# Performance work log

Hardware: AMD Instinct MI355X
Metric: run time of the kernel (lower is better)

## Reference

```python
import jax, jax.numpy as jnp
import numpy as np

LN_EPS = 1e-5

def _layernorm(x, gamma, beta):
    # x: [B, 4, H]; gamma/beta: [4, H]; computed in fp32 as the torch subclass does
    x32 = x.astype(jnp.float32)
    mu = jnp.mean(x32, axis=-1, keepdims=True)
    var = jnp.mean(jnp.square(x32 - mu), axis=-1, keepdims=True)
    y = (x32 - mu) * jax.lax.rsqrt(var + LN_EPS)
    return (y * gamma + beta).astype(x.dtype)

def setup_inputs() -> dict:
    key = jax.random.key(0)
    ks = jax.random.split(key, 6)
    B, I, H = 8192, 512, 1024
    x = jax.random.normal(ks[0], (B, I), dtype=jnp.float32)
    h = jax.random.normal(ks[1], (B, H), dtype=jnp.float32)
    c = jax.random.normal(ks[2], (B, H), dtype=jnp.float32)
    Wi = jax.random.normal(ks[3], (I, 4 * H), dtype=jnp.float32) * (1.0 / np.sqrt(I))
    Wh = jax.random.normal(ks[4], (H, 4 * H), dtype=jnp.float32) * (1.0 / np.sqrt(H))
    bh = jax.random.normal(ks[5], (4 * H,), dtype=jnp.float32) * 0.01
    ln_gamma = jnp.ones((4, H), dtype=jnp.float32)
    ln_beta = jnp.zeros((4, H), dtype=jnp.float32)
    return {"x": x, "h": h, "c": c, "Wi": Wi, "Wh": Wh, "bh": bh,
            "ln_gamma": ln_gamma, "ln_beta": ln_beta}

def reference(x, h, c, Wi, Wh, bh, ln_gamma, ln_beta):
    B = x.shape[0]
    H = h.shape[-1]
    gates = x @ Wi + h @ Wh + bh            # [B, 4H]
    gates = gates.reshape(B, 4, H)           # chunk into i, f, g, o
    gates = _layernorm(gates, ln_gamma, ln_beta)
    i, f, g, o = gates[:, 0], gates[:, 1], gates[:, 2], gates[:, 3]
    c_new = jax.nn.sigmoid(f) * c + jax.nn.sigmoid(i) * jnp.tanh(g)
    h_new = jax.nn.sigmoid(o) * jnp.tanh(c_new)   # layer_norm_c is Identity
    return (h_new, c_new)
```

## Files before the change

### kernel.cpp

```cpp
#include <hip/hip_runtime.h>
#include <stdint.h>

#define BATCH 8192
#define IDIM  512
#define HDIM  1024
#define KDIM  1536
#define NDIM  4096
#define BK    32

typedef __bf16 bf16x8 __attribute__((ext_vector_type(8)));
typedef float  f32x4  __attribute__((ext_vector_type(4)));
typedef unsigned short u16x8 __attribute__((ext_vector_type(8)));

__device__ __forceinline__ unsigned short f2bf(float f) {
    union { float f; unsigned u; } v; v.f = f;
    unsigned r = v.u + 0x7fffu + ((v.u >> 16) & 1u);
    return (unsigned short)(r >> 16);
}
__device__ __forceinline__ float bf2f(unsigned short u) {
    union { unsigned u; float f; } v; v.u = ((unsigned)u) << 16;
    return v.f;
}
__device__ __forceinline__ float fexp(float x) {
    return __builtin_amdgcn_exp2f(x * 1.44269504f);
}
__device__ __forceinline__ float sigm(float x) {
    return __builtin_amdgcn_rcpf(1.f + fexp(-x));
}
__device__ __forceinline__ float ftanh(float x) {
    return 1.f - 2.f * __builtin_amdgcn_rcpf(1.f + fexp(2.f * x));
}

__device__ __forceinline__ void load16(void* lds, const void* g) {
    __builtin_amdgcn_global_load_lds(
        (const __attribute__((address_space(1))) unsigned int*)g,
        (__attribute__((address_space(3))) unsigned int*)lds, 16, 0, 0);
}

#define PACKA_BLKS (BATCH * KDIM / 8 / 512)
#define PACKW_BLKS ((NDIM / 64) * (KDIM / 32))
__global__ __launch_bounds__(512) void pack_ab(const float* __restrict__ x,
                                               const float* __restrict__ h,
                                               const float* __restrict__ Wi,
                                               const float* __restrict__ Wh,
                                               unsigned short* __restrict__ A,
                                               unsigned short* __restrict__ Wt) {
    __shared__ float tile[32][65];
    const int t   = threadIdx.x;
    const int blk = blockIdx.x;
    if (blk < PACKA_BLKS) {
        int idx = blk * 512 + t;
        int row = idx / (KDIM / 8);
        int g8  = idx % (KDIM / 8);
        const float* src = (g8 < IDIM / 8)
                         ? x + (size_t)row * IDIM + g8 * 8
                         : h + (size_t)row * HDIM + (g8 - IDIM / 8) * 8;
        float4 v0 = ((const float4*)src)[0];
        float4 v1 = ((const float4*)src)[1];
        u16x8 o;
        o[0] = f2bf(v0.x); o[1] = f2bf(v0.y); o[2] = f2bf(v0.z); o[3] = f2bf(v0.w);
        o[4] = f2bf(v1.x); o[5] = f2bf(v1.y); o[6] = f2bf(v1.z); o[7] = f2bf(v1.w);
        *(u16x8*)(A + (size_t)idx * 8) = o;
    } else {
        int b  = blk - PACKA_BLKS;
        int n0 = (b & 63) * 64;
        int k0 = (b >> 6) * 32;
        int tx = t & 63, ty = t >> 6;
#pragma unroll
        for (int j = 0; j < 4; j++) {
            int k = k0 + ty + 8 * j;
            float v;
            if (k < IDIM) v = Wi[(size_t)k * NDIM + n0 + tx];
            else          v = Wh[(size_t)(k - IDIM) * NDIM + n0 + tx];
            tile[ty + 8 * j][tx] = v;
        }
        __syncthreads();
        int nl = t >> 3, k4 = (t & 7) * 4;
        ushort4 o;
        o.x = f2bf(tile[k4 + 0][nl]);
        o.y = f2bf(tile[k4 + 1][nl]);
        o.z = f2bf(tile[k4 + 2][nl]);
        o.w = f2bf(tile[k4 + 3][nl]);
        *(ushort4*)(Wt + (size_t)(n0 + nl) * KDIM + k0 + k4) = o;
    }
}

__global__ __launch_bounds__(512, 2) void gemm_bt(const unsigned short* __restrict__ A,
                                                  const unsigned short* __restrict__ Bt,
                                                  unsigned short* __restrict__ C) {
    __shared__ __align__(16) unsigned short smem[65536];

    const int t    = threadIdx.x;
    const int wave = t >> 6;
    const int lane = t & 63;
    const int lrow = lane & 15;
    const int quad = lane >> 4;

    const int bid = blockIdx.x;
    const int xcd = bid & 7;
    const int jj  = bid >> 3;
    const int bm  = (xcd * 4 + (jj & 3)) * 256;
    const int bn  = (jj >> 2) * 256;

    const int wm = (wave & 1) * 128;
    const int wn = (wave >> 1) * 64;

    int srcA[2], srcB[2];
#pragma unroll
    for (int j = 0; j < 2; j++) {
        int q   = t + 512 * j;
        int rp  = q >> 3, s = q & 7;
        int xx  = s ^ (rp & 7);
        int row = 2 * rp + (xx >> 2);
        int kc  = xx & 3;
        srcA[j] = (bm + row) * KDIM + kc * 8;
        srcB[j] = (bn + row) * KDIM + kc * 8;
    }

    int offA[8], offB[4];
#pragma unroll
    for (int mt = 0; mt < 8; mt++) {
        int r = wm + mt * 16 + lrow;
        offA[mt] = (r >> 1) * 64 + (((((r & 1) << 2) | quad) ^ ((r >> 1) & 7)) * 8);
    }
#pragma unroll
    for (int nt = 0; nt < 4; nt++) {
        int r = wn + nt * 16 + lrow;
        offB[nt] = (r >> 1) * 64 + (((((r & 1) << 2) | quad) ^ ((r >> 1) & 7)) * 8);
    }

    f32x4 acc[8][4] = {};

#define STAGE(tt) do {                                              \
    unsigned short* _d = smem + (((tt) & 3) << 14);                 \
    const int _ko = (tt) * 32;                                      \
    load16(_d +          t * 8, A  + (size_t)(srcA[0] + _ko));      \
    load16(_d +  4096 +  t * 8, A  + (size_t)(srcA[1] + _ko));      \
    load16(_d +  8192 +  t * 8, Bt + (size_t)(srcB[0] + _ko));      \
    load16(_d + 12288 +  t * 8, Bt + (size_t)(srcB[1] + _ko));      \
} while (0)

    STAGE(0); STAGE(1); STAGE(2);

    const int NT = KDIM / 32;
    for (int T = 0; T < NT; ++T) {
        if (T < NT - 2)       asm volatile("s_waitcnt vmcnt(8)" ::: "memory");
        else if (T == NT - 2) asm volatile("s_waitcnt vmcnt(4)" ::: "memory");
        else                  asm volatile("s_waitcnt vmcnt(0)" ::: "memory");
        __builtin_amdgcn_s_barrier();
        asm volatile("" ::: "memory");

        const unsigned short* bufA = smem + ((T & 3) << 14);
        const unsigned short* bufB = bufA + 8192;

        bf16x8 a[4], b[4], a2[4];
#pragma unroll
        for (int i = 0; i < 4; i++) a[i] = *(const bf16x8*)(bufA + offA[i]);
#pragma unroll
        for (int i = 0; i < 4; i++) b[i] = *(const bf16x8*)(bufB + offB[i]);
        __builtin_amdgcn_sched_barrier(0);
        if (T + 3 < NT) STAGE(T + 3);
#pragma unroll
        for (int i = 0; i < 4; i++) a2[i] = *(const bf16x8*)(bufA + offA[4 + i]);
        __builtin_amdgcn_sched_barrier(0);

        __builtin_amdgcn_s_setprio(1);
#pragma unroll
        for (int mt = 0; mt < 4; mt++)
#pragma unroll
            for (int nt = 0; nt < 4; nt++)
                acc[mt][nt] = __builtin_amdgcn_mfma_f32_16x16x32_bf16(
                    a[mt], b[nt], acc[mt][nt], 0, 0, 0);
        __builtin_amdgcn_sched_barrier(0);

#pragma unroll
        for (int mt = 0; mt < 4; mt++)
#pragma unroll
            for (int nt = 0; nt < 4; nt++)
                acc[4 + mt][nt] = __builtin_amdgcn_mfma_f32_16x16x32_bf16(
                    a2[mt], b[nt], acc[4 + mt][nt], 0, 0, 0);
        __builtin_amdgcn_s_setprio(0);
        asm volatile("" ::: "memory");
    }
#undef STAGE

#pragma unroll
    for (int mt = 0; mt < 8; mt++)
#pragma unroll
        for (int nt = 0; nt < 4; nt++) {
            int row = bm + wm + mt * 16 + quad * 4;
            int col = bn + wn + nt * 16 + lrow;
#pragma unroll
            for (int r = 0; r < 4; r++)
                C[(size_t)(row + r) * NDIM + col] = f2bf(acc[mt][nt][r]);
        }
}

__global__ __launch_bounds__(512) void lstm_ep(const unsigned short* __restrict__ gates,
                                               const float* __restrict__ bh,
                                               const float* __restrict__ c,
                                               const float* __restrict__ gamma,
                                               const float* __restrict__ beta,
                                               float* __restrict__ out) {
    const int wave = threadIdx.x >> 6;
    const int lane = threadIdx.x & 63;
    const int b    = blockIdx.x * 8 + wave;
    const int col0 = lane * 16;

    const unsigned short* gr = gates + (size_t)b * NDIM;
    float v[4][16];
    float s[4], sq[4];
#pragma unroll
    for (int g = 0; g < 4; g++) {
        const unsigned short* gp = gr + g * HDIM + col0;
        u16x8 ga = *(const u16x8*)gp;
        u16x8 gb = *(const u16x8*)(gp + 8);
        float bb[16];
#pragma unroll
        for (int q = 0; q < 4; q++)
            *(float4*)(bb + 4 * q) = ((const float4*)(bh + g * HDIM + col0))[q];
        float ls = 0.f, lq = 0.f;
#pragma unroll
        for (int j = 0; j < 16; j++) {
            float tv = bf2f(j < 8 ? ga[j] : gb[j - 8]) + bb[j];
            v[g][j] = tv; ls += tv; lq += tv * tv;
        }
        s[g] = ls; sq[g] = lq;
    }
#pragma unroll
    for (int off = 32; off; off >>= 1) {
#pragma unroll
        for (int g = 0; g < 4; g++) {
            s[g]  += __shfl_xor(s[g], off);
            sq[g] += __shfl_xor(sq[g], off);
        }
    }
#pragma unroll
    for (int g = 0; g < 4; g++) {
        const float mu  = s[g] * (1.f / HDIM);
        const float var = sq[g] * (1.f / HDIM) - mu * mu;
        const float rs  = rsqrtf(var + 1e-5f);
        float gm[16], bt[16];
#pragma unroll
        for (int q = 0; q < 4; q++) {
            *(float4*)(gm + 4 * q) = ((const float4*)(gamma + g * HDIM + col0))[q];
            *(float4*)(bt + 4 * q) = ((const float4*)(beta  + g * HDIM + col0))[q];
        }
#pragma unroll
        for (int j = 0; j < 16; j++) {
            float y = (v[g][j] - mu) * rs * gm[j] + bt[j];
            v[g][j] = (g == 2) ? ftanh(y) : sigm(y);
        }
    }
    const size_t base = (size_t)b * HDIM + col0;
#pragma unroll
    for (int q = 0; q < 4; q++) {
        float4 ci = *(const float4*)(c + base + 4 * q);
        float4 cn, hn;
#pragma unroll
        for (int e = 0; e < 4; e++) {
            int j = 4 * q + e;
            float cnv = v[1][j] * ((float*)&ci)[e] + v[0][j] * v[2][j];
            ((float*)&cn)[e] = cnv;
            ((float*)&hn)[e] = v[3][j] * ftanh(cnv);
        }
        *(float4*)(out + base + 4 * q) = hn;
        *(float4*)(out + (size_t)BATCH * HDIM + base + 4 * q) = cn;
    }
}

extern "C" void kernel_launch(void* const* d_in, const int* in_sizes, int n_in,
                              void* d_out, int out_size, void* d_ws, size_t ws_size,
                              hipStream_t stream) {
    const float* x     = (const float*)d_in[0];
    const float* h     = (const float*)d_in[1];
    const float* c     = (const float*)d_in[2];
    const float* Wi    = (const float*)d_in[3];
    const float* Wh    = (const float*)d_in[4];
    const float* bh    = (const float*)d_in[5];
    const float* gamma = (const float*)d_in[6];
    const float* beta  = (const float*)d_in[7];
    float* out = (float*)d_out;

    unsigned short* A  = (unsigned short*)d_ws;
    unsigned short* Wt = (unsigned short*)((char*)d_ws + (size_t)BATCH * KDIM * 2);
    unsigned short* gates = (unsigned short*)((char*)d_ws + (size_t)BATCH * KDIM * 2
                                                          + (size_t)NDIM * KDIM * 2);

    pack_ab<<<PACKA_BLKS + PACKW_BLKS, 512, 0, stream>>>(x, h, Wi, Wh, A, Wt);
    gemm_bt<<<dim3((BATCH / 256) * (NDIM / 256)), 512, 0, stream>>>(A, Wt, gates);
    lstm_ep<<<BATCH / 8, 512, 0, stream>>>(gates, bh, c, gamma, beta, out);
}
```

Before: 301.2 us.

## Fuse pack, GEMM and LSTM epilogue into one persistent cooperative kernel

Replaces the three separate launches (pack, GEMM, epilogue) with one cooperative kernel of 256 persistent blocks. Grid-wide syncs separate the phases, and each block loops over several pack chunks, GEMM tiles and epilogue rows. This removes launch gaps and inter-kernel drain, but adds grid-sync cost. It also caps parallelism at 256 blocks, so each block now handles two GEMM tiles serially and pack and epilogue run with fewer blocks.

```diff
diff --git a/kernel.cpp b/kernel.cpp
--- a/kernel.cpp
+++ b/kernel.cpp
@@ -1,12 +1,15 @@
 #include <hip/hip_runtime.h>
+#include <hip/hip_cooperative_groups.h>
 #include <stdint.h>
+
+namespace cg = cooperative_groups;
 
 #define BATCH 8192
 #define IDIM  512
 #define HDIM  1024
 #define KDIM  1536
 #define NDIM  4096
-#define BK    32
+#define NBLK  256
 
 typedef __bf16 bf16x8 __attribute__((ext_vector_type(8)));
 typedef float  f32x4  __attribute__((ext_vector_type(4)));
@@ -37,19 +40,23 @@
         (__attribute__((address_space(3))) unsigned int*)lds, 16, 0, 0);
 }
 
-#define PACKA_BLKS (BATCH * KDIM / 8 / 512)
-#define PACKW_BLKS ((NDIM / 64) * (KDIM / 32))
-__global__ __launch_bounds__(512) void pack_ab(const float* __restrict__ x,
-                                               const float* __restrict__ h,
-                                               const float* __restrict__ Wi,
-                                               const float* __restrict__ Wh,
-                                               unsigned short* __restrict__ A,
-                                               unsigned short* __restrict__ Wt) {
-    __shared__ float tile[32][65];
+__global__ __launch_bounds__(512, 2) void lstm_fused(
+        const float* __restrict__ x,   const float* __restrict__ h,
+        const float* __restrict__ Wi,  const float* __restrict__ Wh,
+        const float* __restrict__ bh,  const float* __restrict__ c,
+        const float* __restrict__ gamma, const float* __restrict__ beta,
+        unsigned short* __restrict__ A, unsigned short* __restrict__ Wt,
+        unsigned short* __restrict__ gates, float* __restrict__ out) {
+    __shared__ __align__(16) unsigned short smem[65536];
+
     const int t   = threadIdx.x;
-    const int blk = blockIdx.x;
-    if (blk < PACKA_BLKS) {
-        int idx = blk * 512 + t;
+    const int bid = blockIdx.x;
+    const int wave = t >> 6;
+    const int lane = t & 63;
+
+#pragma unroll
+    for (int it = 0; it < 12; ++it) {
+        int idx = bid * 512 + t + it * (NBLK * 512);
         int row = idx / (KDIM / 8);
         int g8  = idx % (KDIM / 8);
         const float* src = (g8 < IDIM / 8)
@@ -61,211 +68,205 @@
         o[0] = f2bf(v0.x); o[1] = f2bf(v0.y); o[2] = f2bf(v0.z); o[3] = f2bf(v0.w);
         o[4] = f2bf(v1.x); o[5] = f2bf(v1.y); o[6] = f2bf(v1.z); o[7] = f2bf(v1.w);
         *(u16x8*)(A + (size_t)idx * 8) = o;
-    } else {
-        int b  = blk - PACKA_BLKS;
-        int n0 = (b & 63) * 64;
-        int k0 = (b >> 6) * 32;
+    }
+    {
+        float (*tile)[65] = (float(*)[65])smem;
         int tx = t & 63, ty = t >> 6;
-#pragma unroll
-        for (int j = 0; j < 4; j++) {
-            int k = k0 + ty + 8 * j;
-            float v;
-            if (k < IDIM) v = Wi[(size_t)k * NDIM + n0 + tx];
-            else          v = Wh[(size_t)(k - IDIM) * NDIM + n0 + tx];
-            tile[ty + 8 * j][tx] = v;
-        }
-        __syncthreads();
         int nl = t >> 3, k4 = (t & 7) * 4;
-        ushort4 o;
-        o.x = f2bf(tile[k4 + 0][nl]);
-        o.y = f2bf(tile[k4 + 1][nl]);
-        o.z = f2bf(tile[k4 + 2][nl]);
-        o.w = f2bf(tile[k4 + 3][nl]);
-        *(ushort4*)(Wt + (size_t)(n0 + nl) * KDIM + k0 + k4) = o;
-    }
-}
-
-__global__ __launch_bounds__(512, 2) void gemm_bt(const unsigned short* __restrict__ A,
-                                                  const unsigned short* __restrict__ Bt,
-                                                  unsigned short* __restrict__ C) {
-    __shared__ __align__(16) unsigned short smem[65536];
-
-    const int t    = threadIdx.x;
-    const int wave = t >> 6;
-    const int lane = t & 63;
-    const int lrow = lane & 15;
-    const int quad = lane >> 4;
-
-    const int bid = blockIdx.x;
-    const int xcd = bid & 7;
-    const int jj  = bid >> 3;
-    const int bm  = (xcd * 4 + (jj & 3)) * 256;
-    const int bn  = (jj >> 2) * 256;
-
-    const int wm = (wave & 1) * 128;
-    const int wn = (wave >> 1) * 64;
-
-    int srcA[2], srcB[2];
-#pragma unroll
-    for (int j = 0; j < 2; j++) {
-        int q   = t + 512 * j;
-        int rp  = q >> 3, s = q & 7;
-        int xx  = s ^ (rp & 7);
-        int row = 2 * rp + (xx >> 2);
-        int kc  = xx & 3;
-        srcA[j] = (bm + row) * KDIM + kc * 8;
-        srcB[j] = (bn + row) * KDIM + kc * 8;
-    }
-
-    int offA[8], offB[4];
-#pragma unroll
-    for (int mt = 0; mt < 8; mt++) {
-        int r = wm + mt * 16 + lrow;
-        offA[mt] = (r >> 1) * 64 + (((((r & 1) << 2) | quad) ^ ((r >> 1) & 7)) * 8);
-    }
-#pragma unroll
-    for (int nt = 0; nt < 4; nt++) {
-        int r = wn + nt * 16 + lrow;
-        offB[nt] = (r >> 1) * 64 + (((((r & 1) << 2) | quad) ^ ((r >> 1) & 7)) * 8);
-    }
-
-    f32x4 acc[8][4] = {};
+        for (int it = 0; it < 12; ++it) {
+            int b  = bid * 12 + it;
+            int n0 = (b & 63) * 64;
+            int k0 = (b >> 6) * 32;
+#pragma unroll
+            for (int j = 0; j < 4; j++) {
+                int k = k0 + ty + 8 * j;
+                float v;
+                if (k < IDIM) v = Wi[(size_t)k * NDIM + n0 + tx];
+                else          v = Wh[(size_t)(k - IDIM) * NDIM + n0 + tx];
+                tile[ty + 8 * j][tx] = v;
+            }
+            __syncthreads();
+            ushort4 o;
+            o.x = f2bf(tile[k4 + 0][nl]);
+            o.y = f2bf(tile[k4 + 1][nl]);
+            o.z = f2bf(tile[k4 + 2][nl]);
+            o.w = f2bf(tile[k4 + 3][nl]);
+            *(ushort4*)(Wt + (size_t)(n0 + nl) * KDIM + k0 + k4) = o;
+            __syncthreads();
+        }
+    }
+
+    cg::this_grid().sync();
+
+    {
+        const int lrow = lane & 15;
+        const int quad = lane >> 4;
+        const int xcd  = bid & 7;
+        const int wm   = (wave & 1) * 128;
+        const int wn   = (wave >> 1) * 64;
+
+        int offA[8], offB[4];
+#pragma unroll
+        for (int mt = 0; mt < 8; mt++) {
+            int r = wm + mt * 16 + lrow;
+            offA[mt] = (r >> 1) * 64 + (((((r & 1) << 2) | quad) ^ ((r >> 1) & 7)) * 8);
+        }
+#pragma unroll
+        for (int nt = 0; nt < 4; nt++) {
+            int r = wn + nt * 16 + lrow;
+            offB[nt] = (r >> 1) * 64 + (((((r & 1) << 2) | quad) ^ ((r >> 1) & 7)) * 8);
+        }
+
+        for (int p = 0; p < 2; ++p) {
+            const int jj = (bid >> 3) + p * 32;
+            const int bm = (xcd * 4 + (jj & 3)) * 256;
+            const int bn = (jj >> 2) * 256;
+
+            int srcA[2], srcB[2];
+#pragma unroll
+            for (int j = 0; j < 2; j++) {
+                int q   = t + 512 * j;
+                int rp  = q >> 3, s = q & 7;
+                int xx  = s ^ (rp & 7);
+                int row = 2 * rp + (xx >> 2);
+                int kc  = xx & 3;
+                srcA[j] = (bm + row) * KDIM + kc * 8;
+                srcB[j] = (bn + row) * KDIM + kc * 8;
+            }
+
+            f32x4 acc[8][4] = {};
 
 #define STAGE(tt) do {                                              \
     unsigned short* _d = smem + (((tt) & 3) << 14);                 \
     const int _ko = (tt) * 32;                                      \
     load16(_d +          t * 8, A  + (size_t)(srcA[0] + _ko));      \
     load16(_d +  4096 +  t * 8, A  + (size_t)(srcA[1] + _ko));      \
-    load16(_d +  8192 +  t * 8, Bt + (size_t)(srcB[0] + _ko));      \
-    load16(_d + 12288 +  t * 8, Bt + (size_t)(srcB[1] + _ko));      \
+    load16(_d +  8192 +  t * 8, Wt + (size_t)(srcB[0] + _ko));      \
+    load16(_d + 12288 +  t * 8, Wt + (size_t)(srcB[1] + _ko));      \
 } while (0)
 
-    STAGE(0); STAGE(1); STAGE(2);
-
-    const int NT = KDIM / 32;
-    for (int T = 0; T < NT; ++T) {
-        if (T < NT - 2)       asm volatile("s_waitcnt vmcnt(8)" ::: "memory");
-        else if (T == NT - 2) asm volatile("s_waitcnt vmcnt(4)" ::: "memory");
-        else                  asm volatile("s_waitcnt vmcnt(0)" ::: "memory");
-        __builtin_amdgcn_s_barrier();
-        asm volatile("" ::: "memory");
-
-        const unsigned short* bufA = smem + ((T & 3) << 14);
-        const unsigned short* bufB = bufA + 8192;
-
-        bf16x8 a[4], b[4], a2[4];
-#pragma unroll
-        for (int i = 0; i < 4; i++) a[i] = *(const bf16x8*)(bufA + offA[i]);
-#pragma unroll
-        for (int i = 0; i < 4; i++) b[i] = *(const bf16x8*)(bufB + offB[i]);
-        __builtin_amdgcn_sched_barrier(0);
-        if (T + 3 < NT) STAGE(T + 3);
-#pragma unroll
-        for (int i = 0; i < 4; i++) a2[i] = *(const bf16x8*)(bufA + offA[4 + i]);
-        __builtin_amdgcn_sched_barrier(0);
-
-        __builtin_amdgcn_s_setprio(1);
-#pragma unroll
-        for (int mt = 0; mt < 4; mt++)
-#pragma unroll
-            for (int nt = 0; nt < 4; nt++)
-                acc[mt][nt] = __builtin_amdgcn_mfma_f32_16x16x32_bf16(
-                    a[mt], b[nt], acc[mt][nt], 0, 0, 0);
-        __builtin_amdgcn_sched_barrier(0);
-
-#pragma unroll
-        for (int mt = 0; mt < 4; mt++)
-#pragma unroll
-            for (int nt = 0; nt < 4; nt++)
-                acc[4 + mt][nt] = __builtin_amdgcn_mfma_f32_16x16x32_bf16(
-                    a2[mt], b[nt], acc[4 + mt][nt], 0, 0, 0);
-        __builtin_amdgcn_s_setprio(0);
-        asm volatile("" ::: "memory");
-    }
+            STAGE(0); STAGE(1); STAGE(2);
+
+            const int NT = KDIM / 32;
+            for (int T = 0; T < NT; ++T) {
+                if (T < NT - 2)       asm volatile("s_waitcnt vmcnt(8)" ::: "memory");
+                else if (T == NT - 2) asm volatile("s_waitcnt vmcnt(4)" ::: "memory");
+                else                  asm volatile("s_waitcnt vmcnt(0)" ::: "memory");
+                __builtin_amdgcn_s_barrier();
+                asm volatile("" ::: "memory");
+
+                const unsigned short* bufA = smem + ((T & 3) << 14);
+                const unsigned short* bufB = bufA + 8192;
+
+                bf16x8 a[4], b[4], a2[4];
+#pragma unroll
+                for (int i = 0; i < 4; i++) a[i] = *(const bf16x8*)(bufA + offA[i]);
+#pragma unroll
+                for (int i = 0; i < 4; i++) b[i] = *(const bf16x8*)(bufB + offB[i]);
+                __builtin_amdgcn_sched_barrier(0);
+                if (T + 3 < NT) STAGE(T + 3);
+#pragma unroll
+                for (int i = 0; i < 4; i++) a2[i] = *(const bf16x8*)(bufA + offA[4 + i]);
+                __builtin_amdgcn_sched_barrier(0);
+
+                __builtin_amdgcn_s_setprio(1);
+#pragma unroll
+                for (int mt = 0; mt < 4; mt++)
+#pragma unroll
+                    for (int nt = 0; nt < 4; nt++)
+                        acc[mt][nt] = __builtin_amdgcn_mfma_f32_16x16x32_bf16(
+                            a[mt], b[nt], acc[mt][nt], 0, 0, 0);
+                __builtin_amdgcn_sched_barrier(0);
+#pragma unroll
+                for (int mt = 0; mt < 4; mt++)
+#pragma unroll
+                    for (int nt = 0; nt < 4; nt++)
+                        acc[4 + mt][nt] = __builtin_amdgcn_mfma_f32_16x16x32_bf16(
+                            a2[mt], b[nt], acc[4 + mt][nt], 0, 0, 0);
+                __builtin_amdgcn_s_setprio(0);
+                asm volatile("" ::: "memory");
+            }
 #undef STAGE
 
 #pragma unroll
-    for (int mt = 0; mt < 8; mt++)
-#pragma unroll
-        for (int nt = 0; nt < 4; nt++) {
-            int row = bm + wm + mt * 16 + quad * 4;
-            int col = bn + wn + nt * 16 + lrow;
-#pragma unroll
-            for (int r = 0; r < 4; r++)
-                C[(size_t)(row + r) * NDIM + col] = f2bf(acc[mt][nt][r]);
-        }
-}
-
-__global__ __launch_bounds__(512) void lstm_ep(const unsigned short* __restrict__ gates,
-                                               const float* __restrict__ bh,
-                                               const float* __restrict__ c,
-                                               const float* __restrict__ gamma,
-                                               const float* __restrict__ beta,
-                                               float* __restrict__ out) {
-    const int wave = threadIdx.x >> 6;
-    const int lane = threadIdx.x & 63;
-    const int b    = blockIdx.x * 8 + wave;
-    const int col0 = lane * 16;
-
-    const unsigned short* gr = gates + (size_t)b * NDIM;
-    float v[4][16];
-    float s[4], sq[4];
-#pragma unroll
-    for (int g = 0; g < 4; g++) {
-        const unsigned short* gp = gr + g * HDIM + col0;
-        u16x8 ga = *(const u16x8*)gp;
-        u16x8 gb = *(const u16x8*)(gp + 8);
-        float bb[16];
-#pragma unroll
-        for (int q = 0; q < 4; q++)
-            *(float4*)(bb + 4 * q) = ((const float4*)(bh + g * HDIM + col0))[q];
-        float ls = 0.f, lq = 0.f;
-#pragma unroll
-        for (int j = 0; j < 16; j++) {
-            float tv = bf2f(j < 8 ? ga[j] : gb[j - 8]) + bb[j];
-            v[g][j] = tv; ls += tv; lq += tv * tv;
-        }
-        s[g] = ls; sq[g] = lq;
-    }
-#pragma unroll
-    for (int off = 32; off; off >>= 1) {
+            for (int mt = 0; mt < 8; mt++)
+#pragma unroll
+                for (int nt = 0; nt < 4; nt++) {
+                    int row = bm + wm + mt * 16 + quad * 4;
+                    int col = bn + wn + nt * 16 + lrow;
+#pragma unroll
+                    for (int r = 0; r < 4; r++)
+                        gates[(size_t)(row + r) * NDIM + col] = f2bf(acc[mt][nt][r]);
+                }
+        }
+    }
+
+    cg::this_grid().sync();
+
+    for (int it = 0; it < 4; ++it) {
+        const int b    = it * (NBLK * 8) + bid * 8 + wave;
+        const int col0 = lane * 16;
+
+        const unsigned short* gr = gates + (size_t)b * NDIM;
+        float v[4][16];
+        float s[4], sq[4];
 #pragma unroll
         for (int g = 0; g < 4; g++) {
-            s[g]  += __shfl_xor(s[g], off);
-            sq[g] += __shfl_xor(sq[g], off);
-        }
-    }
-#pragma unroll
-    for (int g = 0; g < 4; g++) {
-        const float mu  = s[g] * (1.f / HDIM);
-        const float var = sq[g] * (1.f / HDIM) - mu * mu;
-        const float rs  = rsqrtf(var + 1e-5f);
-        float gm[16], bt[16];
+            const unsigned short* gp = gr + g * HDIM + col0;
+            u16x8 ga = *(const u16x8*)gp;
+            u16x8 gb = *(const u16x8*)(gp + 8);
+            float bb[16];
+#pragma unroll
+            for (int q = 0; q < 4; q++)
+                *(float4*)(bb + 4 * q) = ((const float4*)(bh + g * HDIM + col0))[q];
+            float ls = 0.f, lq = 0.f;
+#pragma unroll
+            for (int j = 0; j < 16; j++) {
+                float tv = bf2f(j < 8 ? ga[j] : gb[j - 8]) + bb[j];
+                v[g][j] = tv; ls += tv; lq += tv * tv;
+            }
+            s[g] = ls; sq[g] = lq;
+        }
+#pragma unroll
+        for (int off = 32; off; off >>= 1) {
+#pragma unroll
+            for (int g = 0; g < 4; g++) {
+                s[g]  += __shfl_xor(s[g], off);
+                sq[g] += __shfl_xor(sq[g], off);
+            }
+        }
+#pragma unroll
+        for (int g = 0; g < 4; g++) {
+            const float mu  = s[g] * (1.f / HDIM);
+            const float var = sq[g] * (1.f / HDIM) - mu * mu;
+            const float rs  = rsqrtf(var + 1e-5f);
+            float gm[16], bt[16];
+#pragma unroll
+            for (int q = 0; q < 4; q++) {
+                *(float4*)(gm + 4 * q) = ((const float4*)(gamma + g * HDIM + col0))[q];
+                *(float4*)(bt + 4 * q) = ((const float4*)(beta  + g * HDIM + col0))[q];
+            }
+#pragma unroll
+            for (int j = 0; j < 16; j++) {
+                float y = (v[g][j] - mu) * rs * gm[j] + bt[j];
+                v[g][j] = (g == 2) ? ftanh(y) : sigm(y);
+            }
+        }
+        const size_t base = (size_t)b * HDIM + col0;
 #pragma unroll
         for (int q = 0; q < 4; q++) {
-            *(float4*)(gm + 4 * q) = ((const float4*)(gamma + g * HDIM + col0))[q];
-            *(float4*)(bt + 4 * q) = ((const float4*)(beta  + g * HDIM + col0))[q];
-        }
-#pragma unroll
-        for (int j = 0; j < 16; j++) {
-            float y = (v[g][j] - mu) * rs * gm[j] + bt[j];
-            v[g][j] = (g == 2) ? ftanh(y) : sigm(y);
-        }
-    }
-    const size_t base = (size_t)b * HDIM + col0;
-#pragma unroll
-    for (int q = 0; q < 4; q++) {
-        float4 ci = *(const float4*)(c + base + 4 * q);
-        float4 cn, hn;
-#pragma unroll
-        for (int e = 0; e < 4; e++) {
-            int j = 4 * q + e;
-            float cnv = v[1][j] * ((float*)&ci)[e] + v[0][j] * v[2][j];
-            ((float*)&cn)[e] = cnv;
-            ((float*)&hn)[e] = v[3][j] * ftanh(cnv);
-        }
-        *(float4*)(out + base + 4 * q) = hn;
-        *(float4*)(out + (size_t)BATCH * HDIM + base + 4 * q) = cn;
+            float4 ci = *(const float4*)(c + base + 4 * q);
+            float4 cn, hn;
+#pragma unroll
+            for (int e = 0; e < 4; e++) {
+                int j = 4 * q + e;
+                float cnv = v[1][j] * ((float*)&ci)[e] + v[0][j] * v[2][j];
+                ((float*)&cn)[e] = cnv;
+                ((float*)&hn)[e] = v[3][j] * ftanh(cnv);
+            }
+            *(float4*)(out + base + 4 * q) = hn;
+            *(float4*)(out + (size_t)BATCH * HDIM + base + 4 * q) = cn;
+        }
     }
 }
 
@@ -287,7 +288,9 @@
     unsigned short* gates = (unsigned short*)((char*)d_ws + (size_t)BATCH * KDIM * 2
                                                           + (size_t)NDIM * KDIM * 2);
 
-    pack_ab<<<PACKA_BLKS + PACKW_BLKS, 512, 0, stream>>>(x, h, Wi, Wh, A, Wt);
-    gemm_bt<<<dim3((BATCH / 256) * (NDIM / 256)), 512, 0, stream>>>(A, Wt, gates);
-    lstm_ep<<<BATCH / 8, 512, 0, stream>>>(gates, bh, c, gamma, beta, out);
-}
+    void* args[] = { (void*)&x, (void*)&h, (void*)&Wi, (void*)&Wh,
+                     (void*)&bh, (void*)&c, (void*)&gamma, (void*)&beta,
+                     (void*)&A, (void*)&Wt, (void*)&gates, (void*)&out };
+    hipLaunchCooperativeKernel((const void*)lstm_fused, dim3(NBLK), dim3(512),
+                               args, 0, stream);
+}
```

Result: slower. 423.3 us (+40.5%).
